# Kernel optimization log

Measured on AMD Instinct MI355X. Metric: run time of the kernel, lower is better.

Reference implementation:

```python
import jax, jax.numpy as jnp
import numpy as np

HEAD_DIM = 32
KERNEL = 9
DILATION = 3


def setup_inputs() -> dict:
    key = jax.random.key(0)
    k1, k2, k3 = jax.random.split(key, 3)
    B, d, L = 4, 512, 4096
    q = jax.random.normal(k1, (B, d, 1, L), dtype=jnp.float32)
    k = jax.random.normal(k2, (B, d, 1, L), dtype=jnp.float32)
    v = jax.random.normal(k3, (B, d, 1, L), dtype=jnp.float32)
    return {"q": q, "k": k, "v": v}


def reference(q, k, v):
    # q,k,v: [B, d, 1, L]; output: [B, 1, L, d]
    B, d, _, N = q.shape
    hd = HEAD_DIM
    h = d // hd
    K = KERNEL
    dil = DILATION
    pad = dil * (K - 1) // 2
    scale = hd ** -0.5

    # Window gather indices replicating nn.Unfold with zero padding.
    idx = jnp.arange(N)[:, None] + jnp.arange(K)[None, :] * dil - pad  # [N, K]
    valid = ((idx >= 0) & (idx < N)).astype(q.dtype)                   # [N, K]
    idxc = jnp.clip(idx, 0, N - 1)

    qr = q.reshape(B, h, hd, N)
    kr = k.reshape(B, h, hd, N)
    vr = v.reshape(B, h, hd, N)

    # Unfolded windows: [B, h, hd, N, K], zero outside bounds (like Unfold padding)
    kw = kr[:, :, :, idxc] * valid
    vw = vr[:, :, :, idxc] * valid

    attn = jnp.einsum('bhdn,bhdnk->bhnk', qr, kw) * scale
    attn = jax.nn.softmax(attn, axis=-1)
    out = jnp.einsum('bhnk,bhdnk->bhnd', attn, vw)  # [B, h, N, hd]
    # torch: transpose(1,2).reshape(B,1,N,d) -> heads concatenated per token
    return out.transpose(0, 2, 1, 3).reshape(B, 1, N, d)
```

## Files before the change

### kernel.cpp

```cpp
#include <hip/hip_runtime.h>
#include <math.h>

#define NPOS 4096
#define DCH  512
#define HD   32
#define NH   16
#define KW   9
#define DIL  3
#define PAD  12
#define TILE   128
#define NTILES (NPOS / TILE)
#define SPANT  (TILE + 2*PAD)
#define ROWF4  (SPANT / 4)
#define SLDS   156
#define ROWC   (SLDS / 4)
#define NCHK   (HD * ROWC)
#define CSPL   8
#define CPT    (HD / CSPL)
#define TPT    4
#define WSPAN  28

__device__ __forceinline__ void gload16(const float* g, float* l) {
    __builtin_amdgcn_global_load_lds(
        (const __attribute__((address_space(1))) void*)g,
        (__attribute__((address_space(3))) void*)l,
        16, 0, 0);
}

__device__ __forceinline__ float dpp_sum8(float x) {
    int t;
    t = __builtin_amdgcn_update_dpp(0, __float_as_int(x), 0xB1, 0xF, 0xF, true);
    x += __int_as_float(t);
    t = __builtin_amdgcn_update_dpp(0, __float_as_int(x), 0x4E, 0xF, 0xF, true);
    x += __int_as_float(t);
    t = __builtin_amdgcn_update_dpp(0, __float_as_int(x), 0x141, 0xF, 0xF, true);
    x += __int_as_float(t);
    return x;
}

__global__ __launch_bounds__(256) void dilate_attn_kernel(
    const float* __restrict__ q,
    const float* __restrict__ k,
    const float* __restrict__ v,
    float* __restrict__ out)
{
    __shared__ float kv[2 * HD * SLDS];
    float* const ks = kv;
    float* const vs = kv + HD * SLDS;

    const int bh   = blockIdx.x >> 5;
    const int tile = blockIdx.x & (NTILES - 1);
    const int n0t  = tile * TILE;
    const int ws   = n0t - PAD;

    const size_t cb = (size_t)bh * HD * NPOS;
    const float* kg = k + cb;
    const float* vg = v + cb;
    const float* qg = q + cb;

    const bool easy = (ws >= 0) && (ws + SPANT <= NPOS);

    if (easy) {
#pragma unroll
        for (int it = 0; it < 5; ++it) {
            int c = it * 256 + (int)threadIdx.x;
            if (c < NCHK) {
                int row = c / ROWC;
                int c4  = c - row * ROWC;
                gload16(kg + (size_t)row * NPOS + (ws + c4 * 4),
                        &kv[(size_t)c * 4]);
            }
        }
#pragma unroll
        for (int it = 0; it < 5; ++it) {
            int c = it * 256 + (int)threadIdx.x;
            if (c < NCHK) {
                int row = c / ROWC;
                int c4  = c - row * ROWC;
                gload16(vg + (size_t)row * NPOS + (ws + c4 * 4),
                        &kv[(size_t)(NCHK + c) * 4]);
            }
        }
    } else {
        for (int p = threadIdx.x; p < HD * ROWF4; p += 256) {
            int row = p / ROWF4;
            int c4  = p - row * ROWF4;
            int g0  = ws + c4 * 4;
            const float* kr = kg + (size_t)row * NPOS;
            const float* vr = vg + (size_t)row * NPOS;
            float4 kk, vv;
            if (g0 >= 0 && g0 + 4 <= NPOS) {
                kk = *(const float4*)(kr + g0);
                vv = *(const float4*)(vr + g0);
            } else {
                int i0 = min(max(g0 + 0, 0), NPOS - 1);
                int i1 = min(max(g0 + 1, 0), NPOS - 1);
                int i2 = min(max(g0 + 2, 0), NPOS - 1);
                int i3 = min(max(g0 + 3, 0), NPOS - 1);
                kk = make_float4(kr[i0], kr[i1], kr[i2], kr[i3]);
                vv = make_float4(vr[i0], vr[i1], vr[i2], vr[i3]);
            }
            *(float4*)&ks[row * SLDS + c4 * 4] = kk;
            *(float4*)&vs[row * SLDS + c4 * 4] = vv;
        }
    }

    const int cs = threadIdx.x & (CSPL - 1);
    const int lg = threadIdx.x >> 3;
    const int n0 = n0t + lg * TPT;

    float4 qv[CPT];
#pragma unroll
    for (int i = 0; i < CPT; ++i) {
        int ch = cs * CPT + i;
        qv[i] = *(const float4*)(qg + (size_t)ch * NPOS + n0);
    }

    __syncthreads();

    float s[TPT][KW];
#pragma unroll
    for (int t = 0; t < TPT; ++t)
#pragma unroll
        for (int j = 0; j < KW; ++j) s[t][j] = 0.0f;

#pragma unroll
    for (int i = 0; i < CPT; ++i) {
        int row = cs * CPT + i;
        const float4* wp = (const float4*)&ks[row * SLDS + lg * TPT];
        float w[WSPAN];
#pragma unroll
        for (int u = 0; u < WSPAN / 4; ++u) {
            float4 x = wp[u];
            w[4*u] = x.x; w[4*u+1] = x.y; w[4*u+2] = x.z; w[4*u+3] = x.w;
        }
        float qt[TPT] = {qv[i].x, qv[i].y, qv[i].z, qv[i].w};
#pragma unroll
        for (int t = 0; t < TPT; ++t)
#pragma unroll
            for (int j = 0; j < KW; ++j)
                s[t][j] = fmaf(qt[t], w[t + 3*j], s[t][j]);
    }

#pragma unroll
    for (int t = 0; t < TPT; ++t)
#pragma unroll
        for (int j = 0; j < KW; ++j)
            s[t][j] = dpp_sum8(s[t][j]);

    const float scale = 0.17677669529663687f;
    if (easy) {
#pragma unroll
        for (int t = 0; t < TPT; ++t) {
            float m = -INFINITY;
#pragma unroll
            for (int j = 0; j < KW; ++j) {
                float x = s[t][j] * scale;
                s[t][j] = x;
                m = fmaxf(m, x);
            }
            float sum = 0.0f;
#pragma unroll
            for (int j = 0; j < KW; ++j) {
                float e = __expf(s[t][j] - m);
                s[t][j] = e;
                sum += e;
            }
            float inv = 1.0f / sum;
#pragma unroll
            for (int j = 0; j < KW; ++j) s[t][j] *= inv;
        }
    } else {
#pragma unroll
        for (int t = 0; t < TPT; ++t) {
            float vm[KW];
            float m = -INFINITY;
#pragma unroll
            for (int j = 0; j < KW; ++j) {
                vm[j] = ((unsigned)(n0 + t + 3*j - PAD) < NPOS) ? 1.0f : 0.0f;
                float x = s[t][j] * scale * vm[j];
                s[t][j] = x;
                m = fmaxf(m, x);
            }
            float sum = 0.0f;
#pragma unroll
            for (int j = 0; j < KW; ++j) {
                float e = __expf(s[t][j] - m);
                s[t][j] = e;
                sum += e;
            }
            float inv = 1.0f / sum;
#pragma unroll
            for (int j = 0; j < KW; ++j)
                s[t][j] *= inv * vm[j];
        }
    }

    float o[TPT][CPT];
#pragma unroll
    for (int t = 0; t < TPT; ++t)
#pragma unroll
        for (int i = 0; i < CPT; ++i) o[t][i] = 0.0f;

#pragma unroll
    for (int i = 0; i < CPT; ++i) {
        int row = cs * CPT + i;
        const float4* wp = (const float4*)&vs[row * SLDS + lg * TPT];
        float w[WSPAN];
#pragma unroll
        for (int u = 0; u < WSPAN / 4; ++u) {
            float4 x = wp[u];
            w[4*u] = x.x; w[4*u+1] = x.y; w[4*u+2] = x.z; w[4*u+3] = x.w;
        }
#pragma unroll
        for (int t = 0; t < TPT; ++t)
#pragma unroll
            for (int j = 0; j < KW; ++j)
                o[t][i] = fmaf(s[t][j], w[t + 3*j], o[t][i]);
    }

    const int b  = bh >> 4;
    const int hh = bh & (NH - 1);
#pragma unroll
    for (int t = 0; t < TPT; ++t) {
        float* op = out + ((size_t)(b * NPOS + n0 + t)) * DCH + hh * HD + cs * CPT;
        *(float4*)op = make_float4(o[t][0], o[t][1], o[t][2], o[t][3]);
    }
}

extern "C" void kernel_launch(void* const* d_in, const int* in_sizes, int n_in,
                              void* d_out, int out_size, void* d_ws, size_t ws_size,
                              hipStream_t stream) {
    const float* q = (const float*)d_in[0];
    const float* k = (const float*)d_in[1];
    const float* v = (const float*)d_in[2];
    float* out = (float*)d_out;

    const int grid = 4 * NH * NTILES;
    hipLaunchKernelGGL(dilate_attn_kernel, dim3(grid), dim3(256), 0, stream,
                       q, k, v, out);
}
```

Measured before the change: 142.9 us.

## Split K/V LDS waits to overlap V loads with QK and softmax

```diff
diff --git a/kernel.cpp b/kernel.cpp
--- a/kernel.cpp
+++ b/kernel.cpp
@@ -38,6 +38,59 @@
     return x;
 }
 
+__device__ __forceinline__ void load_w(const float* base, float* w) {
+    const float4* wp = (const float4*)base;
+#pragma unroll
+    for (int u = 0; u < WSPAN / 4; ++u) {
+        float4 x = wp[u];
+        w[4*u] = x.x; w[4*u+1] = x.y; w[4*u+2] = x.z; w[4*u+3] = x.w;
+    }
+}
+
+__device__ __forceinline__ void qk_pass(const float* ksb, int cs, int lg,
+                                        const float4* qv, float s[TPT][KW]) {
+#pragma unroll
+    for (int t = 0; t < TPT; ++t)
+#pragma unroll
+        for (int j = 0; j < KW; ++j) s[t][j] = 0.0f;
+#pragma unroll
+    for (int i = 0; i < CPT; ++i) {
+        int row = cs * CPT + i;
+        float w[WSPAN];
+        load_w(ksb + row * SLDS + lg * TPT, w);
+        float qt[TPT] = {qv[i].x, qv[i].y, qv[i].z, qv[i].w};
+#pragma unroll
+        for (int t = 0; t < TPT; ++t)
+#pragma unroll
+            for (int j = 0; j < KW; ++j)
+                s[t][j] = fmaf(qt[t], w[t + 3*j], s[t][j]);
+    }
+#pragma unroll
+    for (int t = 0; t < TPT; ++t)
+#pragma unroll
+        for (int j = 0; j < KW; ++j)
+            s[t][j] = dpp_sum8(s[t][j]);
+}
+
+__device__ __forceinline__ void pv_pass(const float* vsb, int cs, int lg,
+                                        const float s[TPT][KW], float o[TPT][CPT]) {
+#pragma unroll
+    for (int t = 0; t < TPT; ++t)
+#pragma unroll
+        for (int i = 0; i < CPT; ++i) o[t][i] = 0.0f;
+#pragma unroll
+    for (int i = 0; i < CPT; ++i) {
+        int row = cs * CPT + i;
+        float w[WSPAN];
+        load_w(vsb + row * SLDS + lg * TPT, w);
+#pragma unroll
+        for (int t = 0; t < TPT; ++t)
+#pragma unroll
+            for (int j = 0; j < KW; ++j)
+                o[t][i] = fmaf(s[t][j], w[t + 3*j], o[t][i]);
+    }
+}
+
 __global__ __launch_bounds__(256) void dilate_attn_kernel(
     const float* __restrict__ q,
     const float* __restrict__ k,
@@ -58,19 +111,32 @@
     const float* vg = v + cb;
     const float* qg = q + cb;
 
+    const int cs = threadIdx.x & (CSPL - 1);
+    const int lg = threadIdx.x >> 3;
+    const int n0 = n0t + lg * TPT;
+
     const bool easy = (ws >= 0) && (ws + SPANT <= NPOS);
+    const float scale = 0.17677669529663687f;
+
+    float4 qv[CPT];
+    float  s[TPT][KW];
+    float  o[TPT][CPT];
 
     if (easy) {
+#pragma unroll
+        for (int i = 0; i < CPT; ++i)
+            qv[i] = *(const float4*)(qg + (size_t)(cs * CPT + i) * NPOS + n0);
+        asm volatile("" ::: "memory");
 #pragma unroll
         for (int it = 0; it < 5; ++it) {
             int c = it * 256 + (int)threadIdx.x;
             if (c < NCHK) {
                 int row = c / ROWC;
                 int c4  = c - row * ROWC;
-                gload16(kg + (size_t)row * NPOS + (ws + c4 * 4),
-                        &kv[(size_t)c * 4]);
-            }
-        }
+                gload16(kg + (size_t)row * NPOS + (ws + c4 * 4), &kv[c * 4]);
+            }
+        }
+        asm volatile("" ::: "memory");
 #pragma unroll
         for (int it = 0; it < 5; ++it) {
             int c = it * 256 + (int)threadIdx.x;
@@ -78,9 +144,40 @@
                 int row = c / ROWC;
                 int c4  = c - row * ROWC;
                 gload16(vg + (size_t)row * NPOS + (ws + c4 * 4),
-                        &kv[(size_t)(NCHK + c) * 4]);
-            }
-        }
+                        &kv[(NCHK + c) * 4]);
+            }
+        }
+        asm volatile("s_waitcnt vmcnt(5)" ::: "memory");
+        __builtin_amdgcn_s_barrier();
+        asm volatile("" ::: "memory");
+
+        qk_pass(ks, cs, lg, qv, s);
+#pragma unroll
+        for (int t = 0; t < TPT; ++t) {
+            float m = -INFINITY;
+#pragma unroll
+            for (int j = 0; j < KW; ++j) {
+                float x = s[t][j] * scale;
+                s[t][j] = x;
+                m = fmaxf(m, x);
+            }
+            float sum = 0.0f;
+#pragma unroll
+            for (int j = 0; j < KW; ++j) {
+                float e = __expf(s[t][j] - m);
+                s[t][j] = e;
+                sum += e;
+            }
+            float inv = 1.0f / sum;
+#pragma unroll
+            for (int j = 0; j < KW; ++j) s[t][j] *= inv;
+        }
+
+        asm volatile("s_waitcnt vmcnt(0)" ::: "memory");
+        __builtin_amdgcn_s_barrier();
+        asm volatile("" ::: "memory");
+
+        pv_pass(vs, cs, lg, s, o);
     } else {
         for (int p = threadIdx.x; p < HD * ROWF4; p += 256) {
             int row = p / ROWF4;
@@ -103,74 +200,13 @@
             *(float4*)&ks[row * SLDS + c4 * 4] = kk;
             *(float4*)&vs[row * SLDS + c4 * 4] = vv;
         }
-    }
-
-    const int cs = threadIdx.x & (CSPL - 1);
-    const int lg = threadIdx.x >> 3;
-    const int n0 = n0t + lg * TPT;
-
-    float4 qv[CPT];
-#pragma unroll
-    for (int i = 0; i < CPT; ++i) {
-        int ch = cs * CPT + i;
-        qv[i] = *(const float4*)(qg + (size_t)ch * NPOS + n0);
-    }
-
-    __syncthreads();
-
-    float s[TPT][KW];
-#pragma unroll
-    for (int t = 0; t < TPT; ++t)
-#pragma unroll
-        for (int j = 0; j < KW; ++j) s[t][j] = 0.0f;
-
-#pragma unroll
-    for (int i = 0; i < CPT; ++i) {
-        int row = cs * CPT + i;
-        const float4* wp = (const float4*)&ks[row * SLDS + lg * TPT];
-        float w[WSPAN];
-#pragma unroll
-        for (int u = 0; u < WSPAN / 4; ++u) {
-            float4 x = wp[u];
-            w[4*u] = x.x; w[4*u+1] = x.y; w[4*u+2] = x.z; w[4*u+3] = x.w;
-        }
-        float qt[TPT] = {qv[i].x, qv[i].y, qv[i].z, qv[i].w};
-#pragma unroll
-        for (int t = 0; t < TPT; ++t)
-#pragma unroll
-            for (int j = 0; j < KW; ++j)
-                s[t][j] = fmaf(qt[t], w[t + 3*j], s[t][j]);
-    }
-
-#pragma unroll
-    for (int t = 0; t < TPT; ++t)
-#pragma unroll
-        for (int j = 0; j < KW; ++j)
-            s[t][j] = dpp_sum8(s[t][j]);
-
-    const float scale = 0.17677669529663687f;
-    if (easy) {
-#pragma unroll
-        for (int t = 0; t < TPT; ++t) {
-            float m = -INFINITY;
-#pragma unroll
-            for (int j = 0; j < KW; ++j) {
-                float x = s[t][j] * scale;
-                s[t][j] = x;
-                m = fmaxf(m, x);
-            }
-            float sum = 0.0f;
-#pragma unroll
-            for (int j = 0; j < KW; ++j) {
-                float e = __expf(s[t][j] - m);
-                s[t][j] = e;
-                sum += e;
-            }
-            float inv = 1.0f / sum;
-#pragma unroll
-            for (int j = 0; j < KW; ++j) s[t][j] *= inv;
-        }
-    } else {
+#pragma unroll
+        for (int i = 0; i < CPT; ++i)
+            qv[i] = *(const float4*)(qg + (size_t)(cs * CPT + i) * NPOS + n0);
+
+        __syncthreads();
+
+        qk_pass(ks, cs, lg, qv, s);
 #pragma unroll
         for (int t = 0; t < TPT; ++t) {
             float vm[KW];
@@ -194,29 +230,7 @@
             for (int j = 0; j < KW; ++j)
                 s[t][j] *= inv * vm[j];
         }
-    }
-
-    float o[TPT][CPT];
-#pragma unroll
-    for (int t = 0; t < TPT; ++t)
-#pragma unroll
-        for (int i = 0; i < CPT; ++i) o[t][i] = 0.0f;
-
-#pragma unroll
-    for (int i = 0; i < CPT; ++i) {
-        int row = cs * CPT + i;
-        const float4* wp = (const float4*)&vs[row * SLDS + lg * TPT];
-        float w[WSPAN];
-#pragma unroll
-        for (int u = 0; u < WSPAN / 4; ++u) {
-            float4 x = wp[u];
-            w[4*u] = x.x; w[4*u+1] = x.y; w[4*u+2] = x.z; w[4*u+3] = x.w;
-        }
-#pragma unroll
-        for (int t = 0; t < TPT; ++t)
-#pragma unroll
-            for (int j = 0; j < KW; ++j)
-                o[t][i] = fmaf(s[t][j], w[t + 3*j], o[t][i]);
+        pv_pass(vs, cs, lg, s, o);
     }
 
     const int b  = bh >> 4;
```

Measured after the change: 141.2 us. Within noise of the previous version (-1.2%).

## Read K/V windows directly from global memory instead of staging through LDS

Applied to the files above, without the earlier changes.

```diff
diff --git a/kernel.cpp b/kernel.cpp
--- a/kernel.cpp
+++ b/kernel.cpp
@@ -10,22 +10,11 @@
 #define PAD  12
 #define TILE   128
 #define NTILES (NPOS / TILE)
-#define SPANT  (TILE + 2*PAD)
-#define ROWF4  (SPANT / 4)
-#define SLDS   156
-#define ROWC   (SLDS / 4)
-#define NCHK   (HD * ROWC)
 #define CSPL   8
 #define CPT    (HD / CSPL)
 #define TPT    4
 #define WSPAN  28
-
-__device__ __forceinline__ void gload16(const float* g, float* l) {
-    __builtin_amdgcn_global_load_lds(
-        (const __attribute__((address_space(1))) void*)g,
-        (__attribute__((address_space(3))) void*)l,
-        16, 0, 0);
-}
+#define WCHK   (WSPAN / 4)
 
 __device__ __forceinline__ float dpp_sum8(float x) {
     int t;
@@ -38,85 +27,59 @@
     return x;
 }
 
+__device__ __forceinline__ void load_w_global(const float* base, float* w) {
+    const float4* wp = (const float4*)base;
+#pragma unroll
+    for (int u = 0; u < WCHK; ++u) {
+        float4 x = wp[u];
+        w[4*u] = x.x; w[4*u+1] = x.y; w[4*u+2] = x.z; w[4*u+3] = x.w;
+    }
+}
+
+__device__ __forceinline__ void load_w_clamped(const float* row, int w0, float* w) {
+#pragma unroll
+    for (int u = 0; u < WCHK; ++u) {
+        int g0 = w0 + 4 * u;
+        if (g0 >= 0 && g0 + 4 <= NPOS) {
+            float4 x = *(const float4*)(row + g0);
+            w[4*u] = x.x; w[4*u+1] = x.y; w[4*u+2] = x.z; w[4*u+3] = x.w;
+        } else {
+#pragma unroll
+            for (int e = 0; e < 4; ++e) {
+                int i = min(max(g0 + e, 0), NPOS - 1);
+                w[4*u + e] = row[i];
+            }
+        }
+    }
+}
+
 __global__ __launch_bounds__(256) void dilate_attn_kernel(
     const float* __restrict__ q,
     const float* __restrict__ k,
     const float* __restrict__ v,
     float* __restrict__ out)
 {
-    __shared__ float kv[2 * HD * SLDS];
-    float* const ks = kv;
-    float* const vs = kv + HD * SLDS;
-
     const int bh   = blockIdx.x >> 5;
     const int tile = blockIdx.x & (NTILES - 1);
     const int n0t  = tile * TILE;
-    const int ws   = n0t - PAD;
-
-    const size_t cb = (size_t)bh * HD * NPOS;
-    const float* kg = k + cb;
-    const float* vg = v + cb;
-    const float* qg = q + cb;
-
-    const bool easy = (ws >= 0) && (ws + SPANT <= NPOS);
-
-    if (easy) {
-#pragma unroll
-        for (int it = 0; it < 5; ++it) {
-            int c = it * 256 + (int)threadIdx.x;
-            if (c < NCHK) {
-                int row = c / ROWC;
-                int c4  = c - row * ROWC;
-                gload16(kg + (size_t)row * NPOS + (ws + c4 * 4),
-                        &kv[(size_t)c * 4]);
-            }
-        }
-#pragma unroll
-        for (int it = 0; it < 5; ++it) {
-            int c = it * 256 + (int)threadIdx.x;
-            if (c < NCHK) {
-                int row = c / ROWC;
-                int c4  = c - row * ROWC;
-                gload16(vg + (size_t)row * NPOS + (ws + c4 * 4),
-                        &kv[(size_t)(NCHK + c) * 4]);
-            }
-        }
-    } else {
-        for (int p = threadIdx.x; p < HD * ROWF4; p += 256) {
-            int row = p / ROWF4;
-            int c4  = p - row * ROWF4;
-            int g0  = ws + c4 * 4;
-            const float* kr = kg + (size_t)row * NPOS;
-            const float* vr = vg + (size_t)row * NPOS;
-            float4 kk, vv;
-            if (g0 >= 0 && g0 + 4 <= NPOS) {
-                kk = *(const float4*)(kr + g0);
-                vv = *(const float4*)(vr + g0);
-            } else {
-                int i0 = min(max(g0 + 0, 0), NPOS - 1);
-                int i1 = min(max(g0 + 1, 0), NPOS - 1);
-                int i2 = min(max(g0 + 2, 0), NPOS - 1);
-                int i3 = min(max(g0 + 3, 0), NPOS - 1);
-                kk = make_float4(kr[i0], kr[i1], kr[i2], kr[i3]);
-                vv = make_float4(vr[i0], vr[i1], vr[i2], vr[i3]);
-            }
-            *(float4*)&ks[row * SLDS + c4 * 4] = kk;
-            *(float4*)&vs[row * SLDS + c4 * 4] = vv;
-        }
-    }
 
     const int cs = threadIdx.x & (CSPL - 1);
     const int lg = threadIdx.x >> 3;
     const int n0 = n0t + lg * TPT;
+    const int w0 = n0 - PAD;
+
+    const size_t cb = (size_t)bh * HD * NPOS;
+    const float* qg = q + cb;
+    const float* kg = k + cb;
+    const float* vg = v + cb;
+
+    const bool easy = (w0 >= 0) && (w0 + WSPAN <= NPOS);
+    const float scale = 0.17677669529663687f;
 
     float4 qv[CPT];
 #pragma unroll
-    for (int i = 0; i < CPT; ++i) {
-        int ch = cs * CPT + i;
-        qv[i] = *(const float4*)(qg + (size_t)ch * NPOS + n0);
-    }
-
-    __syncthreads();
+    for (int i = 0; i < CPT; ++i)
+        qv[i] = *(const float4*)(qg + (size_t)(cs * CPT + i) * NPOS + n0);
 
     float s[TPT][KW];
 #pragma unroll
@@ -124,22 +87,30 @@
 #pragma unroll
         for (int j = 0; j < KW; ++j) s[t][j] = 0.0f;
 
-#pragma unroll
-    for (int i = 0; i < CPT; ++i) {
-        int row = cs * CPT + i;
-        const float4* wp = (const float4*)&ks[row * SLDS + lg * TPT];
-        float w[WSPAN];
-#pragma unroll
-        for (int u = 0; u < WSPAN / 4; ++u) {
-            float4 x = wp[u];
-            w[4*u] = x.x; w[4*u+1] = x.y; w[4*u+2] = x.z; w[4*u+3] = x.w;
-        }
-        float qt[TPT] = {qv[i].x, qv[i].y, qv[i].z, qv[i].w};
-#pragma unroll
-        for (int t = 0; t < TPT; ++t)
-#pragma unroll
-            for (int j = 0; j < KW; ++j)
-                s[t][j] = fmaf(qt[t], w[t + 3*j], s[t][j]);
+    if (easy) {
+#pragma unroll
+        for (int i = 0; i < CPT; ++i) {
+            float w[WSPAN];
+            load_w_global(kg + (size_t)(cs * CPT + i) * NPOS + w0, w);
+            float qt[TPT] = {qv[i].x, qv[i].y, qv[i].z, qv[i].w};
+#pragma unroll
+            for (int t = 0; t < TPT; ++t)
+#pragma unroll
+                for (int j = 0; j < KW; ++j)
+                    s[t][j] = fmaf(qt[t], w[t + 3*j], s[t][j]);
+        }
+    } else {
+#pragma unroll
+        for (int i = 0; i < CPT; ++i) {
+            float w[WSPAN];
+            load_w_clamped(kg + (size_t)(cs * CPT + i) * NPOS, w0, w);
+            float qt[TPT] = {qv[i].x, qv[i].y, qv[i].z, qv[i].w};
+#pragma unroll
+            for (int t = 0; t < TPT; ++t)
+#pragma unroll
+                for (int j = 0; j < KW; ++j)
+                    s[t][j] = fmaf(qt[t], w[t + 3*j], s[t][j]);
+        }
     }
 
 #pragma unroll
@@ -148,7 +119,6 @@
         for (int j = 0; j < KW; ++j)
             s[t][j] = dpp_sum8(s[t][j]);
 
-    const float scale = 0.17677669529663687f;
     if (easy) {
 #pragma unroll
         for (int t = 0; t < TPT; ++t) {
@@ -202,21 +172,28 @@
 #pragma unroll
         for (int i = 0; i < CPT; ++i) o[t][i] = 0.0f;
 
-#pragma unroll
-    for (int i = 0; i < CPT; ++i) {
-        int row = cs * CPT + i;
-        const float4* wp = (const float4*)&vs[row * SLDS + lg * TPT];
-        float w[WSPAN];
-#pragma unroll
-        for (int u = 0; u < WSPAN / 4; ++u) {
-            float4 x = wp[u];
-            w[4*u] = x.x; w[4*u+1] = x.y; w[4*u+2] = x.z; w[4*u+3] = x.w;
-        }
-#pragma unroll
-        for (int t = 0; t < TPT; ++t)
-#pragma unroll
-            for (int j = 0; j < KW; ++j)
-                o[t][i] = fmaf(s[t][j], w[t + 3*j], o[t][i]);
+    if (easy) {
+#pragma unroll
+        for (int i = 0; i < CPT; ++i) {
+            float w[WSPAN];
+            load_w_global(vg + (size_t)(cs * CPT + i) * NPOS + w0, w);
+#pragma unroll
+            for (int t = 0; t < TPT; ++t)
+#pragma unroll
+                for (int j = 0; j < KW; ++j)
+                    o[t][i] = fmaf(s[t][j], w[t + 3*j], o[t][i]);
+        }
+    } else {
+#pragma unroll
+        for (int i = 0; i < CPT; ++i) {
+            float w[WSPAN];
+            load_w_clamped(vg + (size_t)(cs * CPT + i) * NPOS, w0, w);
+#pragma unroll
+            for (int t = 0; t < TPT; ++t)
+#pragma unroll
+                for (int j = 0; j < KW; ++j)
+                    o[t][i] = fmaf(s[t][j], w[t + 3*j], o[t][i]);
+        }
     }
 
     const int b  = bh >> 4;
```

Result: slower. 178.5 us (+25.0%).
